# Kernel optimization log

Hardware: AMD Instinct MI355X
Metric: run time of the kernel (lower is better)

The kernel has to match this reference:

```python
import jax, jax.numpy as jnp
import numpy as np

GX, GY = 480, 360  # grid_size
EPS = 1e-5  # BatchNorm eps


def _bn(x, g, b):
    # BatchNorm1d in training mode: batch statistics, biased variance
    m = jnp.mean(x, axis=0)
    v = jnp.var(x, axis=0)
    return (x - m) * jax.lax.rsqrt(v + EPS) * g + b


def setup_inputs() -> dict:
    key = jax.random.key(0)
    ks = jax.random.split(key, 16)
    B, N, F = 2, 200000, 9
    pt_fea = jax.random.normal(ks[0], (B, N, F), dtype=jnp.float32)
    xy_ind = jax.random.randint(ks[1], (B, N, 2), 0, 360, dtype=jnp.int64)

    def lin(k, fi, fo):
        s = 1.0 / np.sqrt(fi)
        kw, kb = jax.random.split(k)
        W = jax.random.uniform(kw, (fi, fo), jnp.float32, -s, s)
        b = jax.random.uniform(kb, (fo,), jnp.float32, -s, s)
        return W, b

    W1, b1 = lin(ks[2], F, 64)
    W2, b2 = lin(ks[3], 64, 128)
    W3, b3 = lin(ks[4], 128, 256)
    W4, b4 = lin(ks[5], 256, 64)
    return {
        "pt_fea": pt_fea, "xy_ind": xy_ind,
        "bn0_g": jnp.ones((F,)), "bn0_b": jnp.zeros((F,)),
        "W1": W1, "b1": b1, "bn1_g": jnp.ones((64,)), "bn1_b": jnp.zeros((64,)),
        "W2": W2, "b2": b2, "bn2_g": jnp.ones((128,)), "bn2_b": jnp.zeros((128,)),
        "W3": W3, "b3": b3, "bn3_g": jnp.ones((256,)), "bn3_b": jnp.zeros((256,)),
        "W4": W4, "b4": b4,
    }


def reference(pt_fea, xy_ind, bn0_g, bn0_b, W1, b1, bn1_g, bn1_b,
              W2, b2, bn2_g, bn2_b, W3, b3, bn3_g, bn3_b, W4, b4):
    B, N, F = pt_fea.shape
    P = B * N  # total points
    x = pt_fea.reshape(P, F)

    # composite voxel key = batch * GX*GY + ix * GY + iy (equivalent to
    # torch.unique over the padded [batch, ix, iy] rows)
    bidx = jnp.repeat(jnp.arange(B, dtype=xy_ind.dtype), N)
    ind = xy_ind.reshape(P, 2)
    keys = bidx * (GX * GY) + ind[:, 0] * GY + ind[:, 1]
    unq_keys, unq_inv = jnp.unique(keys, return_inverse=True, size=P, fill_value=-1)

    # per-point MLP (BN -> Lin -> BN -> ReLU -> ... )
    h = _bn(x, bn0_g, bn0_b)
    h = jax.nn.relu(_bn(h @ W1 + b1, bn1_g, bn1_b))
    h = jax.nn.relu(_bn(h @ W2 + b2, bn2_g, bn2_b))
    h = jax.nn.relu(_bn(h @ W3 + b3, bn3_g, bn3_b))
    h = h @ W4 + b4  # [P, 64]

    # scatter_mean over voxel segments
    sums = jax.ops.segment_sum(h, unq_inv, num_segments=P)
    cnt = jax.ops.segment_sum(jnp.ones((P,), h.dtype), unq_inv, num_segments=P)
    pooled = sums / jnp.maximum(cnt, 1.0)[:, None]

    # decode unique keys back to [batch, ix, iy]; padded slots have key=-1
    ub = unq_keys // (GX * GY)
    rem = unq_keys % (GX * GY)
    unq = jnp.stack([ub, rem // GY, rem % GY], axis=1).astype(jnp.int64)
    return unq, pooled
```

## Files before the change

kernel.cpp:

```cpp
#include <hip/hip_runtime.h>
#include <hip/hip_bf16.h>

#define GXGY 172800
#define GYC  360
#define NKEYS 345600
#define SCAN_NB 338
#define STATS_NBLK 256
#define SQOFF 65536

typedef short short8_t __attribute__((ext_vector_type(8)));
typedef float floatx4 __attribute__((ext_vector_type(4)));

__device__ inline float bf2f(unsigned short u) {
  union { unsigned int i; float f; } v;
  v.i = ((unsigned int)u) << 16;
  return v.f;
}
__device__ inline unsigned short f2bf(float f) {
  union { float f; unsigned int i; } v;
  v.f = f;
  unsigned int lsb = (v.i >> 16) & 1u;
  return (unsigned short)((v.i + 0x7FFFu + lsb) >> 16);
}
__device__ inline unsigned int pk2bf(float lo, float hi) {
  __hip_bfloat162 h = __float22bfloat162_rn(float2{lo, hi});
  union { __hip_bfloat162 h; unsigned int u; } c;
  c.h = h;
  return c.u;
}
__device__ inline unsigned int aff2(unsigned int pr, float a0, float c0, float a1, float c1) {
  union { unsigned int i; float f; } t0, t1;
  t0.i = pr << 16; t1.i = pr & 0xFFFF0000u;
  float v0 = fmaxf(fmaf(t0.f, a0, c0), 0.f);
  float v1 = fmaxf(fmaf(t1.f, a1, c1), 0.f);
  return pk2bf(v0, v1);
}

__global__ __launch_bounds__(1024) void k_detect(const int* __restrict__ xy, int* __restrict__ flag) {
  __shared__ int any;
  if (threadIdx.x == 0) any = 0;
  __syncthreads();
  if (xy[threadIdx.x * 2 + 1] != 0) atomicOr(&any, 1);
  __syncthreads();
  if (threadIdx.x == 0) *flag = any;
}

__device__ inline void load_xy(const int* xy, const int* flag, int p, int& ix, int& iy) {
  if (*flag) { ix = xy[(size_t)p * 2]; iy = xy[(size_t)p * 2 + 1]; }
  else       { ix = xy[(size_t)p * 4]; iy = xy[(size_t)p * 4 + 2]; }
}


__global__ __launch_bounds__(256) void k_count(const int* __restrict__ xy, const int* __restrict__ flag,
                                               int* __restrict__ counts, int P, int N) {
  int p = blockIdx.x * 256 + threadIdx.x;
  if (p >= P) return;
  int ix, iy;
  load_xy(xy, flag, p, ix, iy);
  int key = ((p >= N) ? GXGY : 0) + ix * GYC + iy;
  atomicAdd(&counts[key], 1);
}

__global__ __launch_bounds__(256) void k_scan1b(const int* __restrict__ counts,
                                                int* __restrict__ prefix, int* __restrict__ prefixS,
                                                int* __restrict__ blockTot, int* __restrict__ blockTotS) {
  __shared__ int sf[256], sv[256];
  int base = blockIdx.x * 1024;
  int f[4], c[4];
  int tf = 0, tv = 0;
#pragma unroll
  for (int i = 0; i < 4; ++i) {
    int k = base + threadIdx.x * 4 + i;
    int cnt = (k < NKEYS) ? counts[k] : 0;
    c[i] = cnt;
    f[i] = (cnt > 0) ? 1 : 0;
    tf += f[i];
    tv += c[i];
  }
  sf[threadIdx.x] = tf;
  sv[threadIdx.x] = tv;
  __syncthreads();
  for (int off = 1; off < 256; off <<= 1) {
    int a = (threadIdx.x >= off) ? sf[threadIdx.x - off] : 0;
    int b = (threadIdx.x >= off) ? sv[threadIdx.x - off] : 0;
    __syncthreads();
    if (threadIdx.x >= off) {
      sf[threadIdx.x] += a;
      sv[threadIdx.x] += b;
    }
    __syncthreads();
  }
  int runF = (threadIdx.x == 0) ? 0 : sf[threadIdx.x - 1];
  int runV = (threadIdx.x == 0) ? 0 : sv[threadIdx.x - 1];
#pragma unroll
  for (int i = 0; i < 4; ++i) {
    int k = base + threadIdx.x * 4 + i;
    if (k < NKEYS) {
      prefix[k] = runF;
      prefixS[k] = runV;
    }
    runF += f[i];
    runV += c[i];
  }
  if (threadIdx.x == 255) {
    blockTot[blockIdx.x] = sf[255];
    blockTotS[blockIdx.x] = sv[255];
  }
}

__global__ __launch_bounds__(512) void k_scan2b(const int* __restrict__ blockTot,
                                                const int* __restrict__ blockTotS,
                                                int* __restrict__ blockOff, int* __restrict__ blockOffS,
                                                int* __restrict__ dU) {
  __shared__ int s[512];
  const int* in = (blockIdx.x == 0) ? blockTot : blockTotS;
  int* out = (blockIdx.x == 0) ? blockOff : blockOffS;
  int v = (threadIdx.x < SCAN_NB) ? in[threadIdx.x] : 0;
  s[threadIdx.x] = v;
  __syncthreads();
  for (int off = 1; off < 512; off <<= 1) {
    int t = (threadIdx.x >= off) ? s[threadIdx.x - off] : 0;
    __syncthreads();
    if (threadIdx.x >= off) s[threadIdx.x] += t;
    __syncthreads();
  }
  if (threadIdx.x < SCAN_NB) out[threadIdx.x] = s[threadIdx.x] - v;
  if (blockIdx.x == 0 && threadIdx.x == 511) *dU = s[511];
}

__global__ __launch_bounds__(256) void k_fillpad(int* __restrict__ counts, const int* __restrict__ prefix,
                                                 const int* __restrict__ blockOff,
                                                 const int* __restrict__ prefixS, const int* __restrict__ blockOffS,
                                                 const int* __restrict__ dU,
                                                 float* __restrict__ out_unq, int2* __restrict__ rankCS, int P) {
  int i = blockIdx.x * 256 + threadIdx.x;
  if (i < NKEYS) {
    int cnt = counts[i];
    if (cnt > 0) {
      counts[i] = 0;
      int r = prefix[i] + blockOff[i >> 10];
      rankCS[r] = make_int2(cnt, prefixS[i] + blockOffS[i >> 10]);
      int b = i / GXGY;
      int rem = i % GXGY;
      out_unq[(size_t)r * 3 + 0] = (float)b;
      out_unq[(size_t)r * 3 + 1] = (float)(rem / GYC);
      out_unq[(size_t)r * 3 + 2] = (float)(rem % GYC);
    }
  }
  if (i < P && i >= *dU) {
    out_unq[(size_t)i * 3 + 0] = -1.f;
    out_unq[(size_t)i * 3 + 1] = 479.f;
    out_unq[(size_t)i * 3 + 2] = 359.f;
    rankCS[i] = make_int2(0, 0);
  }
}

__global__ __launch_bounds__(256) void k_sortpts(const int* __restrict__ xy, const int* __restrict__ flag,
                                                 const int* __restrict__ prefixS,
                                                 const int* __restrict__ blockOffS, int* __restrict__ cursor,
                                                 int* __restrict__ sorted, int P, int N) {
  int p = blockIdx.x * 256 + threadIdx.x;
  if (p >= P) return;
  int ix, iy;
  load_xy(xy, flag, p, ix, iy);
  int key = ((p >= N) ? GXGY : 0) + ix * GYC + iy;
  int slot = prefixS[key] + blockOffS[key >> 10] + atomicAdd(&cursor[key], 1);
  sorted[slot] = p;
}


__global__ __launch_bounds__(256) void k_stats9(const float* __restrict__ x, int P, float* __restrict__ partials) {
  float s[9] = {0}, q[9] = {0};
  for (int p = blockIdx.x * 256 + threadIdx.x; p < P; p += STATS_NBLK * 256) {
#pragma unroll
    for (int k = 0; k < 9; ++k) {
      float v = x[(size_t)p * 9 + k];
      s[k] += v;
      q[k] += v * v;
    }
  }
  __shared__ float ls[256 * 9];
#pragma unroll
  for (int k = 0; k < 9; ++k) ls[threadIdx.x * 9 + k] = s[k];
  __syncthreads();
  if (threadIdx.x < 9) {
    float acc = 0;
    for (int t = 0; t < 256; ++t) acc += ls[t * 9 + threadIdx.x];
    partials[blockIdx.x * 9 + threadIdx.x] = acc;
  }
  __syncthreads();
#pragma unroll
  for (int k = 0; k < 9; ++k) ls[threadIdx.x * 9 + k] = q[k];
  __syncthreads();
  if (threadIdx.x < 9) {
    float acc = 0;
    for (int t = 0; t < 256; ++t) acc += ls[t * 9 + threadIdx.x];
    partials[SQOFF + blockIdx.x * 9 + threadIdx.x] = acc;
  }
}

__global__ void k_finalize(const float* __restrict__ partials, const float* __restrict__ gam,
                           const float* __restrict__ bet, float* __restrict__ ac, int F, int P) {
  int f = threadIdx.x;
  if (f >= F) return;
  float s = 0.f, q = 0.f;
  for (int blk = 0; blk < STATS_NBLK; ++blk) {
    s += partials[blk * F + f];
    q += partials[SQOFF + blk * F + f];
  }
  float mean = s / (float)P;
  float var = q / (float)P - mean * mean;
  float A = gam[f] * rsqrtf(var + 1e-5f);
  ac[f] = A;
  ac[256 + f] = bet[f] - mean * A;
}

__global__ void k_finalize_at(const float* __restrict__ stats, const float* __restrict__ gam,
                              const float* __restrict__ bet, float* __restrict__ ac, int F, int P) {
  int f = threadIdx.x;
  if (f >= F) return;
  float mean = stats[f] / (float)P;
  float var = stats[256 + f] / (float)P - mean * mean;
  float A = gam[f] * rsqrtf(var + 1e-5f);
  ac[f] = A;
  ac[256 + f] = bet[f] - mean * A;
}

__global__ __launch_bounds__(256) void k_stage1s(const float* __restrict__ x, const float* __restrict__ ac,
                                                 const float* __restrict__ W1, const float* __restrict__ b1,
                                                 unsigned short* __restrict__ y1, float* __restrict__ stats,
                                                 int P) {
  __shared__ float sW[576];
  __shared__ float sb[64];
  __shared__ float sa[9], sc[9];
  __shared__ float xT[288];
  __shared__ float gS[256], gQ[256];
  const int tid = threadIdx.x;
  for (int i = tid; i < 576; i += 256) sW[i] = W1[i];
  if (tid < 64) sb[tid] = b1[tid];
  if (tid < 9) {
    sa[tid] = ac[tid];
    sc[tid] = ac[256 + tid];
  }
  const int row_l = tid >> 3;
  const int cg = tid & 7;
  const int tiles = P >> 5;
  float sS[8] = {}, sQ[8] = {};
  float pre0 = 0.f, pre1 = 0.f;
  int tile = blockIdx.x;
  if (tile < tiles) {
    size_t base = (size_t)tile * 288;
    pre0 = x[base + tid];
    if (tid < 32) pre1 = x[base + 256 + tid];
  }
  __syncthreads();
  for (; tile < tiles; tile += gridDim.x) {
    xT[tid] = pre0;
    if (tid < 32) xT[256 + tid] = pre1;
    __syncthreads();
    int nt = tile + gridDim.x;
    if (nt < tiles) {
      size_t base = (size_t)nt * 288;
      pre0 = x[base + tid];
      if (tid < 32) pre1 = x[base + 256 + tid];
    }
    float acc[8];
#pragma unroll
    for (int c = 0; c < 8; ++c) acc[c] = sb[cg * 8 + c];
#pragma unroll
    for (int k = 0; k < 9; ++k) {
      float xn = fmaf(xT[row_l * 9 + k], sa[k], sc[k]);
#pragma unroll
      for (int c = 0; c < 8; ++c) acc[c] = fmaf(xn, sW[k * 64 + cg * 8 + c], acc[c]);
    }
    uint4 o;
    o.x = pk2bf(acc[0], acc[1]);
    o.y = pk2bf(acc[2], acc[3]);
    o.z = pk2bf(acc[4], acc[5]);
    o.w = pk2bf(acc[6], acc[7]);
    *(uint4*)&y1[((size_t)tile * 32 + row_l) * 64 + cg * 8] = o;
#pragma unroll
    for (int c = 0; c < 8; ++c) {
      sS[c] += acc[c];
      sQ[c] += acc[c] * acc[c];
    }
    __syncthreads();
  }
#pragma unroll
  for (int c = 0; c < 8; ++c) {
    sS[c] += __shfl_xor(sS[c], 8);
    sS[c] += __shfl_xor(sS[c], 16);
    sS[c] += __shfl_xor(sS[c], 32);
    sQ[c] += __shfl_xor(sQ[c], 8);
    sQ[c] += __shfl_xor(sQ[c], 16);
    sQ[c] += __shfl_xor(sQ[c], 32);
  }
  int lane = tid & 63, wv = tid >> 6;
  if (lane < 8) {
#pragma unroll
    for (int c = 0; c < 8; ++c) {
      gS[wv * 64 + lane * 8 + c] = sS[c];
      gQ[wv * 64 + lane * 8 + c] = sQ[c];
    }
  }
  __syncthreads();
  if (tid < 64) {
    float S = gS[tid] + gS[64 + tid] + gS[128 + tid] + gS[192 + tid];
    float Q = gQ[tid] + gQ[64 + tid] + gQ[128 + tid] + gQ[192 + tid];
    atomicAdd(&stats[tid], S);
    atomicAdd(&stats[256 + tid], Q);
  }
}

template <int K>
__global__ __launch_bounds__(256, 4) void k_gemmM(const unsigned short* __restrict__ X,
                                                  const float* __restrict__ acIn,
                                                  const float* __restrict__ W, const float* __restrict__ bias,
                                                  unsigned short* __restrict__ Y, float* __restrict__ stats,
                                                  int N, int P) {
  constexpr int SEGS = K / 8;
  constexpr int NIT = K / 32;
  constexpr int KPA = K + 8;
  constexpr int OFF_C = 64 * KPA * 2;
  constexpr int OFF_AC = OFF_C + 64 * 136 * 2;
  constexpr int OFF_B = OFF_AC + 512 * 4;
  constexpr int SMEM = OFF_B + 128 * 4;
  static_assert(64 * KPA * 2 + 64 * 136 * 2 >= 128 * KPA * 2, "WTtmp alias fits in A+Csm");
  __shared__ __align__(16) char smem[SMEM];
  unsigned short* A   = (unsigned short*)smem;
  unsigned short* Csm = (unsigned short*)(smem + OFF_C);
  unsigned short* WTt = (unsigned short*)smem;
  float* acL = (float*)(smem + OFF_AC);
  float* bL  = (float*)(smem + OFF_B);

  const int tid = threadIdx.x;
  const int nq = blockIdx.y;

  for (int i = tid; i < 128 * K; i += 256) {
    int k = i >> 7, n = i & 127;
    WTt[n * KPA + k] = f2bf(W[(size_t)k * N + nq * 128 + n]);
  }
  for (int i = tid; i < 512; i += 256) acL[i] = acIn[i];
  if (tid < 128) bL[tid] = bias[nq * 128 + tid];
  __syncthreads();

  const int lane = tid & 63;
  const int w = tid >> 6;
  const int li = lane & 15, lg = lane >> 4;
  const int cb = 32 * w;

  short8_t bfr[2][K / 32];
#pragma unroll
  for (int t = 0; t < 2; ++t)
#pragma unroll
    for (int s = 0; s < K / 32; ++s)
      bfr[t][s] = *(const short8_t*)&WTt[(cb + 16 * t + li) * KPA + 32 * s + 8 * lg];
  __syncthreads();

  const int tiles = P >> 6;
  float sS[2] = {0.f, 0.f}, sQ[2] = {0.f, 0.f};
  uint4 pre[NIT];
  int tile = blockIdx.x;
  if (tile < tiles) {
#pragma unroll
    for (int it = 0; it < NIT; ++it) {
      int i = tid + it * 256;
      int row = i / SEGS, seg = i % SEGS;
      pre[it] = *(const uint4*)&X[((size_t)tile * 64 + row) * K + seg * 8];
    }
  }
  for (; tile < tiles; tile += gridDim.x) {
    const size_t row0 = (size_t)tile * 64;
#pragma unroll
    for (int it = 0; it < NIT; ++it) {
      int i = tid + it * 256;
      int row = i / SEGS, seg = i % SEGS;
      const float* ap = &acL[seg * 8];
      const float* cp = &acL[256 + seg * 8];
      uint4 o;
      o.x = aff2(pre[it].x, ap[0], cp[0], ap[1], cp[1]);
      o.y = aff2(pre[it].y, ap[2], cp[2], ap[3], cp[3]);
      o.z = aff2(pre[it].z, ap[4], cp[4], ap[5], cp[5]);
      o.w = aff2(pre[it].w, ap[6], cp[6], ap[7], cp[7]);
      *(uint4*)&A[row * KPA + seg * 8] = o;
    }
    __syncthreads();
    int nt = tile + gridDim.x;
    if (nt < tiles) {
#pragma unroll
      for (int it = 0; it < NIT; ++it) {
        int i = tid + it * 256;
        int row = i / SEGS, seg = i % SEGS;
        pre[it] = *(const uint4*)&X[((size_t)nt * 64 + row) * K + seg * 8];
      }
    }

    floatx4 acc[4][2];
#pragma unroll
    for (int m = 0; m < 4; ++m)
#pragma unroll
      for (int t = 0; t < 2; ++t) acc[m][t] = (floatx4){0.f, 0.f, 0.f, 0.f};

#pragma unroll
    for (int s = 0; s < K / 32; ++s) {
      const int ko = 32 * s + 8 * lg;
      short8_t af0 = *(const short8_t*)&A[(li) * KPA + ko];
      short8_t af1 = *(const short8_t*)&A[(16 + li) * KPA + ko];
      short8_t af2 = *(const short8_t*)&A[(32 + li) * KPA + ko];
      short8_t af3 = *(const short8_t*)&A[(48 + li) * KPA + ko];
      acc[0][0] = __builtin_amdgcn_mfma_f32_16x16x32_bf16(af0, bfr[0][s], acc[0][0], 0, 0, 0);
      acc[1][0] = __builtin_amdgcn_mfma_f32_16x16x32_bf16(af1, bfr[0][s], acc[1][0], 0, 0, 0);
      acc[2][0] = __builtin_amdgcn_mfma_f32_16x16x32_bf16(af2, bfr[0][s], acc[2][0], 0, 0, 0);
      acc[3][0] = __builtin_amdgcn_mfma_f32_16x16x32_bf16(af3, bfr[0][s], acc[3][0], 0, 0, 0);
      acc[0][1] = __builtin_amdgcn_mfma_f32_16x16x32_bf16(af0, bfr[1][s], acc[0][1], 0, 0, 0);
      acc[1][1] = __builtin_amdgcn_mfma_f32_16x16x32_bf16(af1, bfr[1][s], acc[1][1], 0, 0, 0);
      acc[2][1] = __builtin_amdgcn_mfma_f32_16x16x32_bf16(af2, bfr[1][s], acc[2][1], 0, 0, 0);
      acc[3][1] = __builtin_amdgcn_mfma_f32_16x16x32_bf16(af3, bfr[1][s], acc[3][1], 0, 0, 0);
    }

#pragma unroll
    for (int m = 0; m < 4; ++m)
#pragma unroll
      for (int t = 0; t < 2; ++t) {
        int col = cb + 16 * t + li;
        float bb = bL[col];
#pragma unroll
        for (int rp = 0; rp < 2; ++rp) {
          int rowc = 16 * m + 4 * lg + 2 * rp;
          float v0 = acc[m][t][2 * rp] + bb;
          float v1 = acc[m][t][2 * rp + 1] + bb;
          unsigned int u = pk2bf(v0, v1);
          Csm[rowc * 136 + col] = (unsigned short)(u & 0xFFFFu);
          Csm[(rowc + 1) * 136 + col] = (unsigned short)(u >> 16);
          sS[t] += v0 + v1;
          sQ[t] += v0 * v0 + v1 * v1;
        }
      }
    __syncthreads();
    for (int i = tid; i < 1024; i += 256) {
      int rowc = i >> 4, seg = i & 15;
      *(uint4*)&Y[(row0 + rowc) * N + nq * 128 + seg * 8] = *(const uint4*)&Csm[rowc * 136 + seg * 8];
    }
  }

#pragma unroll
  for (int t = 0; t < 2; ++t) {
    float s = sS[t];
    s += __shfl_xor(s, 16);
    s += __shfl_xor(s, 32);
    float q = sQ[t];
    q += __shfl_xor(q, 16);
    q += __shfl_xor(q, 32);
    if (lane < 16) {
      int col = nq * 128 + cb + 16 * t + li;
      atomicAdd(&stats[col], s);
      atomicAdd(&stats[256 + col], q);
    }
  }
}

__global__ __launch_bounds__(512, 4) void k_gemm3w(const unsigned short* __restrict__ X,
                                                   const float* __restrict__ acIn,
                                                   const float* __restrict__ W, const float* __restrict__ bias,
                                                   unsigned short* __restrict__ Y, float* __restrict__ stats,
                                                   int P) {
  __shared__ __align__(16) char smem[17408 + 33792 + 2048 + 1024];
  unsigned short* A   = (unsigned short*)smem;
  unsigned short* Csm = (unsigned short*)(smem + 17408);
  float* acL = (float*)(smem + 17408 + 33792);
  float* bL  = (float*)(smem + 17408 + 33792 + 2048);

  const int tid = threadIdx.x;
  for (int i = tid; i < 512; i += 512) acL[i] = acIn[i];
  if (tid < 256) bL[tid] = bias[tid];

  const int lane = tid & 63;
  const int w = tid >> 6;
  const int li = lane & 15, lg = lane >> 4;
  const int cb = 32 * w;

  short8_t bfr[2][4];
#pragma unroll
  for (int t = 0; t < 2; ++t)
#pragma unroll
    for (int s = 0; s < 4; ++s) {
      int col = cb + 16 * t + li;
      int kb = 32 * s + 8 * lg;
      unsigned short tmp[8];
#pragma unroll
      for (int j = 0; j < 8; ++j) tmp[j] = f2bf(W[(size_t)(kb + j) * 256 + col]);
      bfr[t][s] = *(const short8_t*)tmp;
    }
  __syncthreads();

  const int tiles = P >> 6;
  float sS[2] = {0.f, 0.f}, sQ[2] = {0.f, 0.f};
  uint4 pre[2];
  int tile = blockIdx.x;
  if (tile < tiles) {
#pragma unroll
    for (int it = 0; it < 2; ++it) {
      int i = tid + it * 512;
      int row = i >> 4, seg = i & 15;
      pre[it] = *(const uint4*)&X[((size_t)tile * 64 + row) * 128 + seg * 8];
    }
  }
  for (; tile < tiles; tile += gridDim.x) {
    const size_t row0 = (size_t)tile * 64;
#pragma unroll
    for (int it = 0; it < 2; ++it) {
      int i = tid + it * 512;
      int row = i >> 4, seg = i & 15;
      const float* ap = &acL[seg * 8];
      const float* cp = &acL[256 + seg * 8];
      uint4 o;
      o.x = aff2(pre[it].x, ap[0], cp[0], ap[1], cp[1]);
      o.y = aff2(pre[it].y, ap[2], cp[2], ap[3], cp[3]);
      o.z = aff2(pre[it].z, ap[4], cp[4], ap[5], cp[5]);
      o.w = aff2(pre[it].w, ap[6], cp[6], ap[7], cp[7]);
      *(uint4*)&A[row * 136 + seg * 8] = o;
    }
    __syncthreads();
    int nt = tile + gridDim.x;
    if (nt < tiles) {
#pragma unroll
      for (int it = 0; it < 2; ++it) {
        int i = tid + it * 512;
        int row = i >> 4, seg = i & 15;
        pre[it] = *(const uint4*)&X[((size_t)nt * 64 + row) * 128 + seg * 8];
      }
    }

    floatx4 acc[4][2];
#pragma unroll
    for (int m = 0; m < 4; ++m)
#pragma unroll
      for (int t = 0; t < 2; ++t) acc[m][t] = (floatx4){0.f, 0.f, 0.f, 0.f};

#pragma unroll
    for (int s = 0; s < 4; ++s) {
      const int ko = 32 * s + 8 * lg;
      short8_t af0 = *(const short8_t*)&A[(li) * 136 + ko];
      short8_t af1 = *(const short8_t*)&A[(16 + li) * 136 + ko];
      short8_t af2 = *(const short8_t*)&A[(32 + li) * 136 + ko];
      short8_t af3 = *(const short8_t*)&A[(48 + li) * 136 + ko];
      acc[0][0] = __builtin_amdgcn_mfma_f32_16x16x32_bf16(af0, bfr[0][s], acc[0][0], 0, 0, 0);
      acc[1][0] = __builtin_amdgcn_mfma_f32_16x16x32_bf16(af1, bfr[0][s], acc[1][0], 0, 0, 0);
      acc[2][0] = __builtin_amdgcn_mfma_f32_16x16x32_bf16(af2, bfr[0][s], acc[2][0], 0, 0, 0);
      acc[3][0] = __builtin_amdgcn_mfma_f32_16x16x32_bf16(af3, bfr[0][s], acc[3][0], 0, 0, 0);
      acc[0][1] = __builtin_amdgcn_mfma_f32_16x16x32_bf16(af0, bfr[1][s], acc[0][1], 0, 0, 0);
      acc[1][1] = __builtin_amdgcn_mfma_f32_16x16x32_bf16(af1, bfr[1][s], acc[1][1], 0, 0, 0);
      acc[2][1] = __builtin_amdgcn_mfma_f32_16x16x32_bf16(af2, bfr[1][s], acc[2][1], 0, 0, 0);
      acc[3][1] = __builtin_amdgcn_mfma_f32_16x16x32_bf16(af3, bfr[1][s], acc[3][1], 0, 0, 0);
    }

#pragma unroll
    for (int m = 0; m < 4; ++m)
#pragma unroll
      for (int t = 0; t < 2; ++t) {
        int col = cb + 16 * t + li;
        float bb = bL[col];
#pragma unroll
        for (int rp = 0; rp < 2; ++rp) {
          int rowc = 16 * m + 4 * lg + 2 * rp;
          float v0 = acc[m][t][2 * rp] + bb;
          float v1 = acc[m][t][2 * rp + 1] + bb;
          unsigned int u = pk2bf(v0, v1);
          Csm[rowc * 264 + col] = (unsigned short)(u & 0xFFFFu);
          Csm[(rowc + 1) * 264 + col] = (unsigned short)(u >> 16);
          sS[t] += v0 + v1;
          sQ[t] += v0 * v0 + v1 * v1;
        }
      }
    __syncthreads();
    for (int i = tid; i < 2048; i += 512) {
      int rowc = i >> 5, seg = i & 31;
      *(uint4*)&Y[(row0 + rowc) * 256 + seg * 8] = *(const uint4*)&Csm[rowc * 264 + seg * 8];
    }
  }

#pragma unroll
  for (int t = 0; t < 2; ++t) {
    float s = sS[t];
    s += __shfl_xor(s, 16);
    s += __shfl_xor(s, 32);
    float q = sQ[t];
    q += __shfl_xor(q, 16);
    q += __shfl_xor(q, 32);
    if (lane < 16) {
      int col = cb + 16 * t + li;
      atomicAdd(&stats[col], s);
      atomicAdd(&stats[256 + col], q);
    }
  }
}

__global__ __launch_bounds__(256, 4) void k_gemm4(const unsigned short* __restrict__ y3,
                                                  const float* __restrict__ ac3,
                                                  const float* __restrict__ W4, const float* __restrict__ b4,
                                                  const int* __restrict__ sorted,
                                                  unsigned short* __restrict__ h4, int P) {
  __shared__ __align__(16) char smem[34816 + 2048 + 256 + 256];
  unsigned short* A0 = (unsigned short*)smem;
  unsigned short* A1 = (unsigned short*)(smem + 17408);
  unsigned short* WTt = (unsigned short*)smem;
  float* acL = (float*)(smem + 34816);
  float* bL  = (float*)(smem + 34816 + 2048);
  int* sIdsL = (int*)(smem + 34816 + 2048 + 256);

  const int tid = threadIdx.x;
  for (int i = tid; i < 64 * 256; i += 256) {
    int k = i >> 6, n = i & 63;
    WTt[n * 264 + k] = f2bf(W4[(size_t)k * 64 + n]);
  }
  for (int i = tid; i < 512; i += 256) acL[i] = ac3[i];
  if (tid < 64) bL[tid] = b4[tid];
  __syncthreads();

  const int lane = tid & 63;
  const int w = tid >> 6;
  const int li = lane & 15, lg = lane >> 4;
  const int cb = 16 * w;
  const int tiles = P >> 6;

  short8_t bfr[8];
#pragma unroll
  for (int s = 0; s < 8; ++s)
    bfr[s] = *(const short8_t*)&WTt[(cb + li) * 264 + 32 * s + 8 * lg];
  __syncthreads();

  int tb = blockIdx.x;
  if (tb >= tiles) return;
  if (tid < 64) sIdsL[tid] = sorted[tb * 64 + tid];
  __syncthreads();

  uint4 preA[4], preB[4];
#pragma unroll
  for (int it = 0; it < 4; ++it) {
    int i = tid + it * 256;
    int row = i >> 4, seg = i & 15;
    preA[it] = *(const uint4*)&y3[(size_t)sIdsL[row] * 256 + seg * 8];
  }

  for (; tb < tiles; tb += gridDim.x) {
    int nt = tb + gridDim.x;
    int sNext = 0;
    if (tid < 64 && nt < tiles) sNext = sorted[nt * 64 + tid];

#pragma unroll
    for (int it = 0; it < 4; ++it) {
      int i = tid + it * 256;
      int row = i >> 4, seg = i & 15;
      const float* ap = &acL[seg * 8];
      const float* cp = &acL[256 + seg * 8];
      uint4 o;
      o.x = aff2(preA[it].x, ap[0], cp[0], ap[1], cp[1]);
      o.y = aff2(preA[it].y, ap[2], cp[2], ap[3], cp[3]);
      o.z = aff2(preA[it].z, ap[4], cp[4], ap[5], cp[5]);
      o.w = aff2(preA[it].w, ap[6], cp[6], ap[7], cp[7]);
      *(uint4*)&A0[row * 136 + seg * 8] = o;
    }
    __syncthreads();

#pragma unroll
    for (int it = 0; it < 4; ++it) {
      int i = tid + it * 256;
      int row = i >> 4, seg = i & 15;
      preB[it] = *(const uint4*)&y3[(size_t)sIdsL[row] * 256 + 128 + seg * 8];
    }

    floatx4 acc[4];
#pragma unroll
    for (int m = 0; m < 4; ++m) acc[m] = (floatx4){0.f, 0.f, 0.f, 0.f};

#pragma unroll
    for (int s = 0; s < 4; ++s) {
      const int ko = 32 * s + 8 * lg;
      short8_t af0 = *(const short8_t*)&A0[(li) * 136 + ko];
      short8_t af1 = *(const short8_t*)&A0[(16 + li) * 136 + ko];
      short8_t af2 = *(const short8_t*)&A0[(32 + li) * 136 + ko];
      short8_t af3 = *(const short8_t*)&A0[(48 + li) * 136 + ko];
      acc[0] = __builtin_amdgcn_mfma_f32_16x16x32_bf16(af0, bfr[s], acc[0], 0, 0, 0);
      acc[1] = __builtin_amdgcn_mfma_f32_16x16x32_bf16(af1, bfr[s], acc[1], 0, 0, 0);
      acc[2] = __builtin_amdgcn_mfma_f32_16x16x32_bf16(af2, bfr[s], acc[2], 0, 0, 0);
      acc[3] = __builtin_amdgcn_mfma_f32_16x16x32_bf16(af3, bfr[s], acc[3], 0, 0, 0);
    }
    __syncthreads();

    if (tid < 64 && nt < tiles) sIdsL[tid] = sNext;
#pragma unroll
    for (int it = 0; it < 4; ++it) {
      int i = tid + it * 256;
      int row = i >> 4, seg = i & 15;
      const float* ap = &acL[128 + seg * 8];
      const float* cp = &acL[256 + 128 + seg * 8];
      uint4 o;
      o.x = aff2(preB[it].x, ap[0], cp[0], ap[1], cp[1]);
      o.y = aff2(preB[it].y, ap[2], cp[2], ap[3], cp[3]);
      o.z = aff2(preB[it].z, ap[4], cp[4], ap[5], cp[5]);
      o.w = aff2(preB[it].w, ap[6], cp[6], ap[7], cp[7]);
      *(uint4*)&A1[row * 136 + seg * 8] = o;
    }
    __syncthreads();

    if (nt < tiles) {
#pragma unroll
      for (int it = 0; it < 4; ++it) {
        int i = tid + it * 256;
        int row = i >> 4, seg = i & 15;
        preA[it] = *(const uint4*)&y3[(size_t)sIdsL[row] * 256 + seg * 8];
      }
    }

#pragma unroll
    for (int s = 0; s < 4; ++s) {
      const int ko = 32 * s + 8 * lg;
      short8_t af0 = *(const short8_t*)&A1[(li) * 136 + ko];
      short8_t af1 = *(const short8_t*)&A1[(16 + li) * 136 + ko];
      short8_t af2 = *(const short8_t*)&A1[(32 + li) * 136 + ko];
      short8_t af3 = *(const short8_t*)&A1[(48 + li) * 136 + ko];
      acc[0] = __builtin_amdgcn_mfma_f32_16x16x32_bf16(af0, bfr[4 + s], acc[0], 0, 0, 0);
      acc[1] = __builtin_amdgcn_mfma_f32_16x16x32_bf16(af1, bfr[4 + s], acc[1], 0, 0, 0);
      acc[2] = __builtin_amdgcn_mfma_f32_16x16x32_bf16(af2, bfr[4 + s], acc[2], 0, 0, 0);
      acc[3] = __builtin_amdgcn_mfma_f32_16x16x32_bf16(af3, bfr[4 + s], acc[3], 0, 0, 0);
    }
    __syncthreads();

    unsigned short* Csm = A1;
    {
      int col = cb + li;
      float bb = bL[col];
#pragma unroll
      for (int m = 0; m < 4; ++m)
#pragma unroll
        for (int rp = 0; rp < 2; ++rp) {
          int rowc = 16 * m + 4 * lg + 2 * rp;
          unsigned int u = pk2bf(acc[m][2 * rp] + bb, acc[m][2 * rp + 1] + bb);
          Csm[rowc * 72 + col] = (unsigned short)(u & 0xFFFFu);
          Csm[(rowc + 1) * 72 + col] = (unsigned short)(u >> 16);
        }
    }
    __syncthreads();
    for (int i = tid; i < 512; i += 256) {
      int rowc = i >> 3, seg = i & 7;
      *(uint4*)&h4[(size_t)(tb * 64 + rowc) * 64 + seg * 8] = *(const uint4*)&Csm[rowc * 72 + seg * 8];
    }
  }
}

__global__ __launch_bounds__(256) void k_gather(const unsigned short* __restrict__ h4,
                                                const int2* __restrict__ rankCS,
                                                float* __restrict__ outp, int P) {
  int wv = threadIdx.x >> 6;
  int j = threadIdx.x & 63;
  int r0 = blockIdx.x * 32 + wv * 8;
  if (r0 >= P) return;
  int cnt[8], st[8];
  int maxc = 0;
#pragma unroll
  for (int i = 0; i < 8; ++i) {
    int2 cs = (r0 + i < P) ? rankCS[r0 + i] : make_int2(0, 0);
    cnt[i] = cs.x;
    st[i] = cs.y;
    maxc = max(maxc, cs.x);
  }
  float acc[8] = {};
  for (int k = 0; k < maxc; ++k) {
#pragma unroll
    for (int i = 0; i < 8; ++i)
      if (k < cnt[i]) acc[i] += bf2f(h4[(size_t)(st[i] + k) * 64 + j]);
  }
#pragma unroll
  for (int i = 0; i < 8; ++i)
    if (r0 + i < P) outp[(size_t)(r0 + i) * 64 + j] = (cnt[i] > 0) ? acc[i] / (float)cnt[i] : 0.f;
}


extern "C" void kernel_launch(void* const* d_in, const int* in_sizes, int n_in,
                              void* d_out, int out_size, void* d_ws, size_t ws_size,
                              hipStream_t stream) {
  const float* pt_fea = (const float*)d_in[0];
  const int*   xy     = (const int*)d_in[1];
  const float* bn0_g = (const float*)d_in[2];
  const float* bn0_b = (const float*)d_in[3];
  const float* W1 = (const float*)d_in[4];
  const float* b1 = (const float*)d_in[5];
  const float* bn1_g = (const float*)d_in[6];
  const float* bn1_b = (const float*)d_in[7];
  const float* W2 = (const float*)d_in[8];
  const float* b2 = (const float*)d_in[9];
  const float* bn2_g = (const float*)d_in[10];
  const float* bn2_b = (const float*)d_in[11];
  const float* W3 = (const float*)d_in[12];
  const float* b3 = (const float*)d_in[13];
  const float* bn3_g = (const float*)d_in[14];
  const float* bn3_b = (const float*)d_in[15];
  const float* W4 = (const float*)d_in[16];
  const float* b4 = (const float*)d_in[17];

  const int P = in_sizes[0] / 9;
  const int Nhalf = P / 2;

  char* w = (char*)d_ws;
  size_t off = 0;
  auto alloc = [&](size_t bytes) -> void* {
    off = (off + 255) & ~(size_t)255;
    void* p = w + off;
    off += bytes;
    return p;
  };
  int* counts    = (int*)alloc((size_t)NKEYS * 4);
  int* prefix    = (int*)alloc((size_t)NKEYS * 4);
  int* prefixS   = (int*)alloc((size_t)NKEYS * 4);
  int* blockTot  = (int*)alloc(512 * 4);
  int* blockOff  = (int*)alloc(512 * 4);
  int* blockTotS = (int*)alloc(512 * 4);
  int* blockOffS = (int*)alloc(512 * 4);
  int* dU        = (int*)alloc(256);
  int* flag      = (int*)alloc(256);
  int2* rankCS   = (int2*)alloc((size_t)P * 8);
  int* sorted    = (int*)alloc((size_t)P * 4);
  float* partials = (float*)alloc((size_t)2 * SQOFF * 4);
  float* st1 = (float*)alloc(512 * 4);
  float* st2 = (float*)alloc(512 * 4);
  float* st3 = (float*)alloc(512 * 4);
  float* ac0 = (float*)alloc(512 * 4);
  float* ac1 = (float*)alloc(512 * 4);
  float* ac2 = (float*)alloc(512 * 4);
  float* ac3 = (float*)alloc(512 * 4);
  unsigned short* y1 = (unsigned short*)alloc((size_t)P * 64 * 2);
  unsigned short* y2 = (unsigned short*)alloc((size_t)P * 128 * 2);
  unsigned short* y3 = (unsigned short*)alloc((size_t)P * 256 * 2);
  (void)ws_size; (void)n_in; (void)out_size;

  float* out_unq = (float*)d_out;
  float* out_pooled = out_unq + (size_t)P * 3;

  const int nbP = (P + 255) / 256;

  hipMemsetAsync(counts, 0, (size_t)NKEYS * 4, stream);
  hipMemsetAsync(st1, 0, 3 * 2048, stream);
  k_detect<<<1, 1024, 0, stream>>>(xy, flag);
  k_count<<<nbP, 256, 0, stream>>>(xy, flag, counts, P, Nhalf);
  k_scan1b<<<SCAN_NB, 256, 0, stream>>>(counts, prefix, prefixS, blockTot, blockTotS);
  k_scan2b<<<2, 512, 0, stream>>>(blockTot, blockTotS, blockOff, blockOffS, dU);
  k_fillpad<<<nbP, 256, 0, stream>>>(counts, prefix, blockOff, prefixS, blockOffS, dU,
                                     out_unq, rankCS, P);
  k_sortpts<<<nbP, 256, 0, stream>>>(xy, flag, prefixS, blockOffS, counts, sorted, P, Nhalf);

  k_stats9<<<STATS_NBLK, 256, 0, stream>>>(pt_fea, P, partials);
  k_finalize<<<1, 9, 0, stream>>>(partials, bn0_g, bn0_b, ac0, 9, P);

  k_stage1s<<<2048, 256, 0, stream>>>(pt_fea, ac0, W1, b1, y1, st1, P);
  k_finalize_at<<<1, 64, 0, stream>>>(st1, bn1_g, bn1_b, ac1, 64, P);

  k_gemmM<64><<<dim3(2048, 1), 256, 0, stream>>>(y1, ac1, W2, b2, y2, st2, 128, P);
  k_finalize_at<<<1, 128, 0, stream>>>(st2, bn2_g, bn2_b, ac2, 128, P);

  k_gemm3w<<<1024, 512, 0, stream>>>(y2, ac2, W3, b3, y3, st3, P);
  k_finalize_at<<<1, 256, 0, stream>>>(st3, bn3_g, bn3_b, ac3, 256, P);

  unsigned short* h4 = y1;
  k_gemm4<<<2048, 256, 0, stream>>>(y3, ac3, W4, b4, sorted, h4, P);

  k_gather<<<(P + 31) / 32, 256, 0, stream>>>(h4, rankCS, out_pooled, P);
}
```

Measured before the change: 392.7 us.

## Recompute layer-3 GEMM instead of materializing y3; fuse with layer-4 GEMM

The layer-3 GEMM now runs only to gather batch-norm statistics, without writing the 256-wide activation. A new fused kernel recomputes layer 3 from y2 for gathered sorted rows, applies BN3 and ReLU, and feeds layer 4 directly through shared memory, splitting K across wave halves and reducing partial sums in LDS. This removes writing and re-reading the large y3 buffer at the cost of doing the layer-3 matmul twice, and lowers occupancy in the fused kernel.

```diff
diff --git a/kernel.cpp b/kernel.cpp
--- a/kernel.cpp
+++ b/kernel.cpp
@@ -459,19 +459,17 @@
   }
 }
 
-__global__ __launch_bounds__(512, 4) void k_gemm3w(const unsigned short* __restrict__ X,
-                                                   const float* __restrict__ acIn,
-                                                   const float* __restrict__ W, const float* __restrict__ bias,
-                                                   unsigned short* __restrict__ Y, float* __restrict__ stats,
-                                                   int P) {
-  __shared__ __align__(16) char smem[17408 + 33792 + 2048 + 1024];
-  unsigned short* A   = (unsigned short*)smem;
-  unsigned short* Csm = (unsigned short*)(smem + 17408);
-  float* acL = (float*)(smem + 17408 + 33792);
-  float* bL  = (float*)(smem + 17408 + 33792 + 2048);
+__global__ __launch_bounds__(512, 4) void k_g3s(const unsigned short* __restrict__ X,
+                                                const float* __restrict__ acIn,
+                                                const float* __restrict__ W, const float* __restrict__ bias,
+                                                float* __restrict__ stats, int P) {
+  __shared__ __align__(16) char smem[17408 + 2048 + 1024];
+  unsigned short* A = (unsigned short*)smem;
+  float* acL = (float*)(smem + 17408);
+  float* bL  = (float*)(smem + 17408 + 2048);
 
   const int tid = threadIdx.x;
-  for (int i = tid; i < 512; i += 512) acL[i] = acIn[i];
+  acL[tid] = acIn[tid & 511];
   if (tid < 256) bL[tid] = bias[tid];
 
   const int lane = tid & 63;
@@ -506,7 +504,6 @@
     }
   }
   for (; tile < tiles; tile += gridDim.x) {
-    const size_t row0 = (size_t)tile * 64;
 #pragma unroll
     for (int it = 0; it < 2; ++it) {
       int i = tid + it * 512;
@@ -558,25 +555,15 @@
     for (int m = 0; m < 4; ++m)
 #pragma unroll
       for (int t = 0; t < 2; ++t) {
-        int col = cb + 16 * t + li;
-        float bb = bL[col];
-#pragma unroll
-        for (int rp = 0; rp < 2; ++rp) {
-          int rowc = 16 * m + 4 * lg + 2 * rp;
-          float v0 = acc[m][t][2 * rp] + bb;
-          float v1 = acc[m][t][2 * rp + 1] + bb;
-          unsigned int u = pk2bf(v0, v1);
-          Csm[rowc * 264 + col] = (unsigned short)(u & 0xFFFFu);
-          Csm[(rowc + 1) * 264 + col] = (unsigned short)(u >> 16);
-          sS[t] += v0 + v1;
-          sQ[t] += v0 * v0 + v1 * v1;
+        float bb = bL[cb + 16 * t + li];
+#pragma unroll
+        for (int r = 0; r < 4; ++r) {
+          float v = acc[m][t][r] + bb;
+          sS[t] += v;
+          sQ[t] += v * v;
         }
       }
     __syncthreads();
-    for (int i = tid; i < 2048; i += 512) {
-      int rowc = i >> 5, seg = i & 31;
-      *(uint4*)&Y[(row0 + rowc) * 256 + seg * 8] = *(const uint4*)&Csm[rowc * 264 + seg * 8];
-    }
   }
 
 #pragma unroll
@@ -595,51 +582,77 @@
   }
 }
 
-__global__ __launch_bounds__(256, 4) void k_gemm4(const unsigned short* __restrict__ y3,
-                                                  const float* __restrict__ ac3,
-                                                  const float* __restrict__ W4, const float* __restrict__ b4,
-                                                  const int* __restrict__ sorted,
-                                                  unsigned short* __restrict__ h4, int P) {
-  __shared__ __align__(16) char smem[34816 + 2048 + 256 + 256];
-  unsigned short* A0 = (unsigned short*)smem;
-  unsigned short* A1 = (unsigned short*)(smem + 17408);
-  unsigned short* WTt = (unsigned short*)smem;
-  float* acL = (float*)(smem + 34816);
-  float* bL  = (float*)(smem + 34816 + 2048);
-  int* sIdsL = (int*)(smem + 34816 + 2048 + 256);
+#define G34_OFF_X4  17408
+#define G34_OFF_AC2 51200
+#define G34_OFF_AC3 53248
+#define G34_OFF_B4  55296
+#define G34_OFF_SID 55552
+#define G34_SMEM    55808
+__global__ __launch_bounds__(512, 2) void k_g34(const unsigned short* __restrict__ y2,
+                                                const float* __restrict__ ac2,
+                                                const float* __restrict__ W3, const float* __restrict__ b3,
+                                                const float* __restrict__ ac3,
+                                                const float* __restrict__ W4, const float* __restrict__ b4,
+                                                const int* __restrict__ sorted,
+                                                unsigned short* __restrict__ h4, int P) {
+  __shared__ __align__(16) char smem[G34_SMEM];
+  unsigned short* A  = (unsigned short*)smem;
+  unsigned short* X4 = (unsigned short*)(smem + G34_OFF_X4);
+  float* acL2 = (float*)(smem + G34_OFF_AC2);
+  float* acL3 = (float*)(smem + G34_OFF_AC3);
+  float* b4L  = (float*)(smem + G34_OFF_B4);
+  int* sIdsL  = (int*)(smem + G34_OFF_SID);
 
   const int tid = threadIdx.x;
-  for (int i = tid; i < 64 * 256; i += 256) {
-    int k = i >> 6, n = i & 63;
-    WTt[n * 264 + k] = f2bf(W4[(size_t)k * 64 + n]);
-  }
-  for (int i = tid; i < 512; i += 256) acL[i] = ac3[i];
-  if (tid < 64) bL[tid] = b4[tid];
-  __syncthreads();
+  acL2[tid] = ac2[tid & 511];
+  if (tid < 256) {
+    float a = ac3[tid];
+    acL3[tid] = a;
+    acL3[256 + tid] = fmaf(a, b3[tid], ac3[256 + tid]);
+  }
+  if (tid < 64) b4L[tid] = b4[tid];
 
   const int lane = tid & 63;
   const int w = tid >> 6;
   const int li = lane & 15, lg = lane >> 4;
-  const int cb = 16 * w;
+  const int cb = 32 * w;
+  const int cg = w & 3, kh = w >> 2;
+
+  short8_t bfr3[2][4];
+#pragma unroll
+  for (int t = 0; t < 2; ++t)
+#pragma unroll
+    for (int s = 0; s < 4; ++s) {
+      int col = cb + 16 * t + li;
+      int kb = 32 * s + 8 * lg;
+      unsigned short tmp[8];
+#pragma unroll
+      for (int j = 0; j < 8; ++j) tmp[j] = f2bf(W3[(size_t)(kb + j) * 256 + col]);
+      bfr3[t][s] = *(const short8_t*)tmp;
+    }
+  short8_t bfr4[4];
+#pragma unroll
+  for (int s = 0; s < 4; ++s) {
+    int col = cg * 16 + li;
+    int kb = kh * 128 + 32 * s + 8 * lg;
+    unsigned short tmp[8];
+#pragma unroll
+    for (int j = 0; j < 8; ++j) tmp[j] = f2bf(W4[(size_t)(kb + j) * 64 + col]);
+    bfr4[s] = *(const short8_t*)tmp;
+  }
+
   const int tiles = P >> 6;
-
-  short8_t bfr[8];
-#pragma unroll
-  for (int s = 0; s < 8; ++s)
-    bfr[s] = *(const short8_t*)&WTt[(cb + li) * 264 + 32 * s + 8 * lg];
-  __syncthreads();
-
   int tb = blockIdx.x;
   if (tb >= tiles) return;
   if (tid < 64) sIdsL[tid] = sorted[tb * 64 + tid];
   __syncthreads();
 
-  uint4 preA[4], preB[4];
-#pragma unroll
-  for (int it = 0; it < 4; ++it) {
-    int i = tid + it * 256;
+  uint4 preA[2];
+#pragma unroll
+  for (int it = 0; it < 2; ++it) {
+    int i = tid + it * 512;
     int row = i >> 4, seg = i & 15;
-    preA[it] = *(const uint4*)&y3[(size_t)sIdsL[row] * 256 + seg * 8];
+    preA[it] = *(const uint4*)&y2[(size_t)sIdsL[row] * 128 + seg * 8];
   }
 
   for (; tb < tiles; tb += gridDim.x) {
@@ -648,102 +661,120 @@
     if (tid < 64 && nt < tiles) sNext = sorted[nt * 64 + tid];
 
 #pragma unroll
-    for (int it = 0; it < 4; ++it) {
-      int i = tid + it * 256;
+    for (int it = 0; it < 2; ++it) {
+      int i = tid + it * 512;
       int row = i >> 4, seg = i & 15;
-      const float* ap = &acL[seg * 8];
-      const float* cp = &acL[256 + seg * 8];
+      const float* ap = &acL2[seg * 8];
+      const float* cp = &acL2[256 + seg * 8];
       uint4 o;
       o.x = aff2(preA[it].x, ap[0], cp[0], ap[1], cp[1]);
       o.y = aff2(preA[it].y, ap[2], cp[2], ap[3], cp[3]);
       o.z = aff2(preA[it].z, ap[4], cp[4], ap[5], cp[5]);
       o.w = aff2(preA[it].w, ap[6], cp[6], ap[7], cp[7]);
-      *(uint4*)&A0[row * 136 + seg * 8] = o;
-    }
-    __syncthreads();
-
-#pragma unroll
-    for (int it = 0; it < 4; ++it) {
-      int i = tid + it * 256;
-      int row = i >> 4, seg = i & 15;
-      preB[it] = *(const uint4*)&y3[(size_t)sIdsL[row] * 256 + 128 + seg * 8];
-    }
-
-    floatx4 acc[4];
-#pragma unroll
-    for (int m = 0; m < 4; ++m) acc[m] = (floatx4){0.f, 0.f, 0.f, 0.f};
-
+      *(uint4*)&A[row * 136 + seg * 8] = o;
+    }
+    __syncthreads();
+    if (tid < 64 && nt < tiles) sIdsL[tid] = sNext;
+
+    floatx4 acc3[4][2];
+#pragma unroll
+    for (int m = 0; m < 4; ++m)
+#pragma unroll
+      for (int t = 0; t < 2; ++t) acc3[m][t] = (floatx4){0.f, 0.f, 0.f, 0.f};
 #pragma unroll
     for (int s = 0; s < 4; ++s) {
       const int ko = 32 * s + 8 * lg;
-      short8_t af0 = *(const short8_t*)&A0[(li) * 136 + ko];
-      short8_t af1 = *(const short8_t*)&A0[(16 + li) * 136 + ko];
-      short8_t af2 = *(const short8_t*)&A0[(32 + li) * 136 + ko];
-      short8_t af3 = *(const short8_t*)&A0[(48 + li) * 136 + ko];
-      acc[0] = __builtin_amdgcn_mfma_f32_16x16x32_bf16(af0, bfr[s], acc[0], 0, 0, 0);
-      acc[1] = __builtin_amdgcn_mfma_f32_16x16x32_bf16(af1, bfr[s], acc[1], 0, 0, 0);
-      acc[2] = __builtin_amdgcn_mfma_f32_16x16x32_bf16(af2, bfr[s], acc[2], 0, 0, 0);
-      acc[3] = __builtin_amdgcn_mfma_f32_16x16x32_bf16(af3, bfr[s], acc[3], 0, 0, 0);
-    }
-    __syncthreads();
-
-    if (tid < 64 && nt < tiles) sIdsL[tid] = sNext;
-#pragma unroll
-    for (int it = 0; it < 4; ++it) {
-      int i = tid + it * 256;
-      int row = i >> 4, seg = i & 15;
-      const float* ap = &acL[128 + seg * 8];
-      const float* cp = &acL[256 + 128 + seg * 8];
-      uint4 o;
-      o.x = aff2(preB[it].x, ap[0], cp[0], ap[1], cp[1]);
-      o.y = aff2(preB[it].y, ap[2], cp[2], ap[3], cp[3]);
-      o.z = aff2(preB[it].z, ap[4], cp[4], ap[5], cp[5]);
-      o.w = aff2(preB[it].w, ap[6], cp[6], ap[7], cp[7]);
-      *(uint4*)&A1[row * 136 + seg * 8] = o;
-    }
-    __syncthreads();
-
-    if (nt < tiles) {
-#pragma unroll
-      for (int it = 0; it < 4; ++it) {
-        int i = tid + it * 256;
-        int row = i >> 4, seg = i & 15;
-        preA[it] = *(const uint4*)&y3[(size_t)sIdsL[row] * 256 + seg * 8];
-      }
-    }
-
-#pragma unroll
-    for (int s = 0; s < 4; ++s) {
-      const int ko = 32 * s + 8 * lg;
-      short8_t af0 = *(const short8_t*)&A1[(li) * 136 + ko];
-      short8_t af1 = *(const short8_t*)&A1[(16 + li) * 136 + ko];
-      short8_t af2 = *(const short8_t*)&A1[(32 + li) * 136 + ko];
-      short8_t af3 = *(const short8_t*)&A1[(48 + li) * 136 + ko];
-      acc[0] = __builtin_amdgcn_mfma_f32_16x16x32_bf16(af0, bfr[4 + s], acc[0], 0, 0, 0);
-      acc[1] = __builtin_amdgcn_mfma_f32_16x16x32_bf16(af1, bfr[4 + s], acc[1], 0, 0, 0);
-      acc[2] = __builtin_amdgcn_mfma_f32_16x16x32_bf16(af2, bfr[4 + s], acc[2], 0, 0, 0);
-      acc[3] = __builtin_amdgcn_mfma_f32_16x16x32_bf16(af3, bfr[4 + s], acc[3], 0, 0, 0);
-    }
-    __syncthreads();
-
-    unsigned short* Csm = A1;
-    {
-      int col = cb + li;
-      float bb = bL[col];
-#pragma unroll
-      for (int m = 0; m < 4; ++m)
+      short8_t af0 = *(const short8_t*)&A[(li) * 136 + ko];
+      short8_t af1 = *(const short8_t*)&A[(16 + li) * 136 + ko];
+      short8_t af2 = *(const short8_t*)&A[(32 + li) * 136 + ko];
+      short8_t af3 = *(const short8_t*)&A[(48 + li) * 136 + ko];
+      acc3[0][0] = __builtin_amdgcn_mfma_f32_16x16x32_bf16(af0, bfr3[0][s], acc3[0][0], 0, 0, 0);
+      acc3[1][0] = __builtin_amdgcn_mfma_f32_16x16x32_bf16(af1, bfr3[0][s], acc3[1][0], 0, 0, 0);
+      acc3[2][0] = __builtin_amdgcn_mfma_f32_16x16x32_bf16(af2, bfr3[0][s], acc3[2][0], 0, 0, 0);
+      acc3[3][0] = __builtin_amdgcn_mfma_f32_16x16x32_bf16(af3, bfr3[0][s], acc3[3][0], 0, 0, 0);
+      acc3[0][1] = __builtin_amdgcn_mfma_f32_16x16x32_bf16(af0, bfr3[1][s], acc3[0][1], 0, 0, 0);
+      acc3[1][1] = __builtin_amdgcn_mfma_f32_16x16x32_bf16(af1, bfr3[1][s], acc3[1][1], 0, 0, 0);
+      acc3[2][1] = __builtin_amdgcn_mfma_f32_16x16x32_bf16(af2, bfr3[1][s], acc3[2][1], 0, 0, 0);
+      acc3[3][1] = __builtin_amdgcn_mfma_f32_16x16x32_bf16(af3, bfr3[1][s], acc3[3][1], 0, 0, 0);
+    }
+
+#pragma unroll
+    for (int m = 0; m < 4; ++m)
+#pragma unroll
+      for (int t = 0; t < 2; ++t) {
+        int col = cb + 16 * t + li;
+        float a3 = acL3[col], c3p = acL3[256 + col];
 #pragma unroll
         for (int rp = 0; rp < 2; ++rp) {
           int rowc = 16 * m + 4 * lg + 2 * rp;
-          unsigned int u = pk2bf(acc[m][2 * rp] + bb, acc[m][2 * rp + 1] + bb);
+          float v0 = fmaxf(fmaf(acc3[m][t][2 * rp], a3, c3p), 0.f);
+          float v1 = fmaxf(fmaf(acc3[m][t][2 * rp + 1], a3, c3p), 0.f);
+          unsigned int u = pk2bf(v0, v1);
+          X4[rowc * 264 + col] = (unsigned short)(u & 0xFFFFu);
+          X4[(rowc + 1) * 264 + col] = (unsigned short)(u >> 16);
+        }
+      }
+    __syncthreads();
+
+    if (nt < tiles) {
+#pragma unroll
+      for (int it = 0; it < 2; ++it) {
+        int i = tid + it * 512;
+        int row = i >> 4, seg = i & 15;
+        preA[it] = *(const uint4*)&y2[(size_t)sIdsL[row] * 128 + seg * 8];
+      }
+    }
+
+    floatx4 acc4[4];
+#pragma unroll
+    for (int m = 0; m < 4; ++m) acc4[m] = (floatx4){0.f, 0.f, 0.f, 0.f};
+#pragma unroll
+    for (int s = 0; s < 4; ++s) {
+      const int ko = kh * 128 + 32 * s + 8 * lg;
+      short8_t af0 = *(const short8_t*)&X4[(li) * 264 + ko];
+      short8_t af1 = *(const short8_t*)&X4[(16 + li) * 264 + ko];
+      short8_t af2 = *(const short8_t*)&X4[(32 + li) * 264 + ko];
+      short8_t af3 = *(const short8_t*)&X4[(48 + li) * 264 + ko];
+      acc4[0] = __builtin_amdgcn_mfma_f32_16x16x32_bf16(af0, bfr4[s], acc4[0], 0, 0, 0);
+      acc4[1] = __builtin_amdgcn_mfma_f32_16x16x32_bf16(af1, bfr4[s], acc4[1], 0, 0, 0);
+      acc4[2] = __builtin_amdgcn_mfma_f32_16x16x32_bf16(af2, bfr4[s], acc4[2], 0, 0, 0);
+      acc4[3] = __builtin_amdgcn_mfma_f32_16x16x32_bf16(af3, bfr4[s], acc4[3], 0, 0, 0);
+    }
+
+    if (w >= 4) {
+      float* part = (float*)smem;
+#pragma unroll
+      for (int m = 0; m < 4; ++m)
+#pragma unroll
+        for (int r = 0; r < 4; ++r) {
+          int rowc = 16 * m + 4 * lg + r;
+          part[cg * 1024 + rowc * 16 + li] = acc4[m][r];
+        }
+    }
+    __syncthreads();
+
+    unsigned short* Csm = X4;
+    if (w < 4) {
+      const float* part = (const float*)smem;
+      int col = cg * 16 + li;
+      float bb = b4L[col];
+#pragma unroll
+      for (int m = 0; m < 4; ++m)
+#pragma unroll
+        for (int rp = 0; rp < 2; ++rp) {
+          int rowc = 16 * m + 4 * lg + 2 * rp;
+          float v0 = acc4[m][2 * rp] + part[cg * 1024 + rowc * 16 + li] + bb;
+          float v1 = acc4[m][2 * rp + 1] + part[cg * 1024 + (rowc + 1) * 16 + li] + bb;
+          unsigned int u = pk2bf(v0, v1);
           Csm[rowc * 72 + col] = (unsigned short)(u & 0xFFFFu);
           Csm[(rowc + 1) * 72 + col] = (unsigned short)(u >> 16);
         }
     }
     __syncthreads();
-    for (int i = tid; i < 512; i += 256) {
-      int rowc = i >> 3, seg = i & 7;
-      *(uint4*)&h4[(size_t)(tb * 64 + rowc) * 64 + seg * 8] = *(const uint4*)&Csm[rowc * 72 + seg * 8];
+
+    {
+      int rowc = tid >> 3, seg = tid & 7;
+      *(uint4*)&h4[((size_t)tb * 64 + rowc) * 64 + seg * 8] = *(const uint4*)&Csm[rowc * 72 + seg * 8];
     }
   }
 }
@@ -830,7 +861,6 @@
   float* ac3 = (float*)alloc(512 * 4);
   unsigned short* y1 = (unsigned short*)alloc((size_t)P * 64 * 2);
   unsigned short* y2 = (unsigned short*)alloc((size_t)P * 128 * 2);
-  unsigned short* y3 = (unsigned short*)alloc((size_t)P * 256 * 2);
   (void)ws_size; (void)n_in; (void)out_size;
 
   float* out_unq = (float*)d_out;
@@ -857,11 +887,11 @@
   k_gemmM<64><<<dim3(2048, 1), 256, 0, stream>>>(y1, ac1, W2, b2, y2, st2, 128, P);
   k_finalize_at<<<1, 128, 0, stream>>>(st2, bn2_g, bn2_b, ac2, 128, P);
 
-  k_gemm3w<<<1024, 512, 0, stream>>>(y2, ac2, W3, b3, y3, st3, P);
+  k_g3s<<<2048, 512, 0, stream>>>(y2, ac2, W3, b3, st3, P);
   k_finalize_at<<<1, 256, 0, stream>>>(st3, bn3_g, bn3_b, ac3, 256, P);
 
   unsigned short* h4 = y1;
-  k_gemm4<<<2048, 256, 0, stream>>>(y3, ac3, W4, b4, sorted, h4, P);
+  k_g34<<<1024, 512, 0, stream>>>(y2, ac2, W3, b3, ac3, W4, b4, sorted, h4, P);
 
   k_gather<<<(P + 31) / 32, 256, 0, stream>>>(h4, rankCS, out_pooled, P);
 }
```

Result: slower. 403.2 us (+2.7%).
